# Performance work log

Measured on AMD Instinct MI355X. Metric: run time of the kernel, lower is better.

## Reference

```python
import jax, jax.numpy as jnp
import numpy as np

N, K, C, H = 8192, 32, 192, 6
HD = C // H                       # head dim = 32
SCALE = HD ** -0.5
POS_BND = int(0.8 * K)            # 25 (OctFormer RPE: 0.8*patch_size*dilation**0.5, dilation=1)
RPE_NUM = 2 * POS_BND + 1         # 51
HID = 4 * C                       # mlp hidden


def setup_inputs() -> dict:
    key = jax.random.key(0)
    ks = jax.random.split(key, 18)
    w = lambda k, sh: (jax.random.normal(k, sh, jnp.float32) * 0.02)
    data = jax.random.normal(ks[0], (N, K, C), jnp.float32)
    # rel_pos: integer xyz offsets between points in a window, roughly in [-32, 32)
    rel_pos = jax.random.randint(ks[1], (N, K, K, 3), 0, 64, jnp.int32) - 32
    mask = jnp.where(jax.random.uniform(ks[2], (N, K, K)) < 0.05, -1e9, 0.0).astype(jnp.float32)
    return {
        "data": data,
        "mask": mask,
        "rel_pos": rel_pos,
        "ln1_g": jnp.ones((C,), jnp.float32),
        "ln1_b": jnp.zeros((C,), jnp.float32),
        "qkv_w": w(ks[3], (C, 3 * C)),
        "qkv_b": jnp.zeros((3 * C,), jnp.float32),
        "rpe_table": w(ks[4], (3 * RPE_NUM, H)),
        "proj_w": w(ks[5], (C, C)),
        "proj_b": jnp.zeros((C,), jnp.float32),
        "ln2_g": jnp.ones((C,), jnp.float32),
        "ln2_b": jnp.zeros((C,), jnp.float32),
        "mlp_w1": w(ks[6], (C, HID)),
        "mlp_b1": jnp.zeros((HID,), jnp.float32),
        "mlp_w2": w(ks[7], (HID, C)),
        "mlp_b2": jnp.zeros((C,), jnp.float32),
    }


def _layernorm(x, g, b):
    m = x.mean(-1, keepdims=True)
    v = ((x - m) ** 2).mean(-1, keepdims=True)
    return (x - m) * jax.lax.rsqrt(v + 1e-5) * g + b


def reference(data, mask, rel_pos, ln1_g, ln1_b, qkv_w, qkv_b, rpe_table,
              proj_w, proj_b, ln2_g, ln2_b, mlp_w1, mlp_b1, mlp_w2, mlp_b2):
    # --- windowed attention (OctreeAttention) ---
    x = _layernorm(data, ln1_g, ln1_b)                      # (N,K,C)
    qkv = (x @ qkv_w + qkv_b).reshape(N, K, 3, H, HD)
    qkv = qkv.transpose(2, 0, 3, 1, 4)                      # (3,N,H,K,HD)
    q, k, v = qkv[0] * SCALE, qkv[1], qkv[2]
    attn = jnp.einsum('nhqd,nhkd->nhqk', q, k)              # (N,H,K,K)
    # RPE: clamp xyz offsets, index per-axis rows of the table, sum over xyz
    idx = jnp.clip(rel_pos, -POS_BND, POS_BND) + POS_BND + jnp.arange(3, dtype=rel_pos.dtype) * RPE_NUM
    rpe = rpe_table[idx].sum(axis=3)                        # (N,K,K,H)
    attn = attn + rpe.transpose(0, 3, 1, 2) + mask[:, None, :, :]
    attn = jax.nn.softmax(attn, axis=-1)
    out = jnp.einsum('nhqk,nhkd->nqhd', attn, v).reshape(N, K, C)
    out = out @ proj_w + proj_b
    data = data + out                                       # residual (gamma1=1, drop_path=0)
    # --- MLP ---
    y = _layernorm(data, ln2_g, ln2_b)
    y = jax.nn.gelu(y @ mlp_w1 + mlp_b1, approximate=False) @ mlp_w2 + mlp_b2
    return data + y
```

## Files before the change

### kernel.cpp

```cpp
#include <hip/hip_runtime.h>
#include <hip/hip_bf16.h>
#include <cmath>


#define KW    32
#define CD    192
#define NH    6
#define HID   768
#define SCALE 0.17677669529663687f

typedef short short8 __attribute__((ext_vector_type(8)));
typedef float f32x4  __attribute__((ext_vector_type(4)));
typedef unsigned short u16;

#define FB_QKV  0
#define FB_PROJ 216
#define FB_MLP1 288
#define FB_MLP2 576
#define NFRAG   864
#define WS_BYTES (NFRAG * 512 * 2)

__device__ __forceinline__ u16 f2bb(float v) {
  __hip_bfloat16 h = __float2bfloat16(v);
  return *(u16*)&h;
}
__device__ __forceinline__ float bb2f(u16 b) {
  union { float f; unsigned u; } x; x.u = ((unsigned)b) << 16; return x.f;
}

__global__ __launch_bounds__(256) void pack_weights(
    const float* __restrict__ qkv_w, const float* __restrict__ proj_w,
    const float* __restrict__ mlp_w1, const float* __restrict__ mlp_w2,
    u16* __restrict__ ws)
{
  const int idx  = blockIdx.x * 256 + threadIdx.x;
  const int f    = idx >> 6;
  const int lane = idx & 63;
  const float* src; int N, KB, fl;
  if (f < FB_PROJ)      { src = qkv_w;  N = 576; KB = 6;  fl = f; }
  else if (f < FB_MLP1) { src = proj_w; N = 192; KB = 6;  fl = f - FB_PROJ; }
  else if (f < FB_MLP2) { src = mlp_w1; N = 768; KB = 6;  fl = f - FB_MLP1; }
  else                  { src = mlp_w2; N = 192; KB = 24; fl = f - FB_MLP2; }
  const int nt = fl / KB, kb = fl % KB;
  const int k0 = kb * 32 + (lane >> 4) * 8;
  const int n  = nt * 16 + (lane & 15);
  u16* dst = ws + ((size_t)(f * 64 + lane)) * 8;
  #pragma unroll
  for (int j = 0; j < 8; ++j) dst[j] = f2bb(src[(size_t)(k0 + j) * N + n]);
}

__global__ __launch_bounds__(512, 4) void octformer_mfma(
    const float* __restrict__ data, const float* __restrict__ mask,
    const int* __restrict__ rel_pos,
    const float* __restrict__ ln1_g, const float* __restrict__ ln1_b,
    const float* __restrict__ qkv_b, const float* __restrict__ rpe_table,
    const float* __restrict__ proj_b,
    const float* __restrict__ ln2_g, const float* __restrict__ ln2_b,
    const float* __restrict__ mlp_b1, const float* __restrict__ mlp_b2,
    const u16* __restrict__ wsb, float* __restrict__ out)
{
  __shared__ __align__(16) u16 s_x[64][200];
  __shared__ __align__(16) u16 s_qkv[64][200];
  __shared__ __align__(16) u16 s_ao[64][200];

  const int tid  = threadIdx.x;
  const int n0   = blockIdx.x * 2;
  const size_t base = (size_t)blockIdx.x * (2 * KW * CD);

  const int wv   = tid >> 6;
  const int lane = tid & 63;
  const int l15  = lane & 15;
  const int quad = lane >> 4;

  const int rg = tid >> 5;
  const int c0 = tid & 31;

  const int mh   = wv >> 2;
  const int nsub = wv & 3;

  const int hh   = wv & 1;
  const int w_at = (wv >> 1) & 1;
  const int rth  = wv >> 2;

  const f32x4 zed = {0.f, 0.f, 0.f, 0.f};

  float res[4][6];
  #pragma unroll
  for (int i = 0; i < 4; ++i) {
    const int r = rg * 4 + i;
    float s = 0.f, q = 0.f;
    #pragma unroll
    for (int j = 0; j < 6; ++j) {
      const float v = data[base + r * CD + c0 + 32 * j];
      res[i][j] = v; s += v; q += v * v;
    }
    #pragma unroll
    for (int m = 16; m >= 1; m >>= 1) { s += __shfl_xor(s, m); q += __shfl_xor(q, m); }
    const float mean = s * (1.0f / CD);
    const float rstd = rsqrtf(q * (1.0f / CD) - mean * mean + 1e-5f);
    #pragma unroll
    for (int j = 0; j < 6; ++j) {
      const int c = c0 + 32 * j;
      s_x[r][c] = f2bb((res[i][j] - mean) * rstd * ln1_g[c] + ln1_b[c]);
    }
  }

  unsigned pidx[2][4];
  #pragma unroll
  for (int ct = 0; ct < 2; ++ct)
    #pragma unroll
    for (int i = 0; i < 4; ++i) {
      const int r = rth * 16 + quad * 4 + i;
      const int c = ct * 16 + l15;
      const size_t g = ((size_t)(n0 + w_at) * KW + r) * KW + c;
      const int* rp = rel_pos + 3 * g;
      int i0 = rp[0]; i0 = i0 < -25 ? -25 : (i0 > 25 ? 25 : i0); i0 += 25;
      int i1 = rp[1]; i1 = i1 < -25 ? -25 : (i1 > 25 ? 25 : i1); i1 += 76;
      int i2 = rp[2]; i2 = i2 < -25 ? -25 : (i2 > 25 ? 25 : i2); i2 += 127;
      const unsigned mb = (mask[g] < -0.5f) ? (1u << 24) : 0u;
      pidx[ct][i] = (unsigned)i0 | ((unsigned)i1 << 8) | ((unsigned)i2 << 16) | mb;
    }
  __syncthreads();

  for (int hp = 0; hp < 3; ++hp) {
    {
      f32x4 acc[3][2];
      #pragma unroll
      for (int ni = 0; ni < 3; ++ni)
        #pragma unroll
        for (int mi = 0; mi < 2; ++mi) acc[ni][mi] = zed;
      for (int kb = 0; kb < 6; ++kb) {
        short8 a[2];
        #pragma unroll
        for (int mi = 0; mi < 2; ++mi)
          a[mi] = *(const short8*)&s_x[(mh * 2 + mi) * 16 + l15][kb * 32 + quad * 8];
        #pragma unroll
        for (int ni = 0; ni < 3; ++ni) {
          const int lnt = nsub + 4 * ni, part = lnt >> 2, sub = lnt & 3;
          const int gnt = part * 12 + hp * 4 + sub;
          const short8 b = *(const short8*)(wsb + ((size_t)((FB_QKV + gnt * 6 + kb) * 64 + lane)) * 8);
          #pragma unroll
          for (int mi = 0; mi < 2; ++mi)
            acc[ni][mi] = __builtin_amdgcn_mfma_f32_16x16x32_bf16(a[mi], b, acc[ni][mi], 0, 0, 0);
        }
      }
      #pragma unroll
      for (int ni = 0; ni < 3; ++ni) {
        const int lnt = nsub + 4 * ni, part = lnt >> 2, sub = lnt & 3;
        const int gnt = part * 12 + hp * 4 + sub;
        const float bias = qkv_b[gnt * 16 + l15];
        if (part < 2) {
          #pragma unroll
          for (int mi = 0; mi < 2; ++mi)
            #pragma unroll
            for (int i = 0; i < 4; ++i) {
              float v = acc[ni][mi][i] + bias;
              if (part == 0) v *= SCALE;
              s_qkv[(mh * 2 + mi) * 16 + quad * 4 + i][part * 64 + sub * 16 + l15] = f2bb(v);
            }
        } else {
          const int vr = (sub >> 1) * 32 + (sub & 1) * 16 + l15;
          #pragma unroll
          for (int mi = 0; mi < 2; ++mi)
            #pragma unroll
            for (int i = 0; i < 4; ++i) {
              const int gr = (mh * 2 + mi) * 16 + quad * 4 + i;
              s_qkv[vr][128 + (gr >> 5) * 32 + (gr & 31)] = f2bb(acc[ni][mi][i] + bias);
            }
        }
      }
    }
    __syncthreads();

    {
      const int h = hp * 2 + hh;
      const int rbase = w_at * 32;
      const short8 qf  = *(const short8*)&s_qkv[rbase + rth * 16 + l15][hh * 32 + quad * 8];
      const short8 kf0 = *(const short8*)&s_qkv[rbase + l15][64 + hh * 32 + quad * 8];
      const short8 kf1 = *(const short8*)&s_qkv[rbase + 16 + l15][64 + hh * 32 + quad * 8];
      const f32x4 sa0 = __builtin_amdgcn_mfma_f32_16x16x32_bf16(qf, kf0, zed, 0, 0, 0);
      const f32x4 sa1 = __builtin_amdgcn_mfma_f32_16x16x32_bf16(qf, kf1, zed, 0, 0, 0);
      float S0[4], S1[4];
      #pragma unroll
      for (int i = 0; i < 4; ++i) {
        unsigned p = pidx[0][i];
        float b = rpe_table[(p & 255u) * NH + h]
                + rpe_table[((p >> 8) & 255u) * NH + h]
                + rpe_table[((p >> 16) & 255u) * NH + h];
        if (p >> 24) b -= 1e9f;
        S0[i] = sa0[i] + b;
        p = pidx[1][i];
        b = rpe_table[(p & 255u) * NH + h]
          + rpe_table[((p >> 8) & 255u) * NH + h]
          + rpe_table[((p >> 16) & 255u) * NH + h];
        if (p >> 24) b -= 1e9f;
        S1[i] = sa1[i] + b;
      }
      #pragma unroll
      for (int i = 0; i < 4; ++i) {
        float mx = fmaxf(S0[i], S1[i]);
        #pragma unroll
        for (int m = 8; m >= 1; m >>= 1) mx = fmaxf(mx, __shfl_xor(mx, m));
        const float e0 = __expf(S0[i] - mx);
        const float e1 = __expf(S1[i] - mx);
        float sm = e0 + e1;
        #pragma unroll
        for (int m = 8; m >= 1; m >>= 1) sm += __shfl_xor(sm, m);
        const float inv = 1.0f / sm;
        const int r = rbase + rth * 16 + quad * 4 + i;
        s_qkv[r][hh * 32 + l15]      = f2bb(e0 * inv);
        s_qkv[r][hh * 32 + 16 + l15] = f2bb(e1 * inv);
      }
      const short8 pf  = *(const short8*)&s_qkv[rbase + rth * 16 + l15][hh * 32 + quad * 8];
      const short8 vf0 = *(const short8*)&s_qkv[hh * 32 + l15][128 + w_at * 32 + quad * 8];
      const short8 vf1 = *(const short8*)&s_qkv[hh * 32 + 16 + l15][128 + w_at * 32 + quad * 8];
      const f32x4 o0 = __builtin_amdgcn_mfma_f32_16x16x32_bf16(pf, vf0, zed, 0, 0, 0);
      const f32x4 o1 = __builtin_amdgcn_mfma_f32_16x16x32_bf16(pf, vf1, zed, 0, 0, 0);
      #pragma unroll
      for (int i = 0; i < 4; ++i) {
        const int r = rbase + rth * 16 + quad * 4 + i;
        s_ao[r][h * 32 + l15]      = f2bb(o0[i]);
        s_ao[r][h * 32 + 16 + l15] = f2bb(o1[i]);
      }
    }
    __syncthreads();
  }

  {
    f32x4 acc[3][2];
    #pragma unroll
    for (int ni = 0; ni < 3; ++ni)
      #pragma unroll
      for (int mi = 0; mi < 2; ++mi) acc[ni][mi] = zed;
    for (int kb = 0; kb < 6; ++kb) {
      short8 a[2];
      #pragma unroll
      for (int mi = 0; mi < 2; ++mi)
        a[mi] = *(const short8*)&s_ao[(mh * 2 + mi) * 16 + l15][kb * 32 + quad * 8];
      #pragma unroll
      for (int ni = 0; ni < 3; ++ni) {
        const int nt = nsub + 4 * ni;
        const short8 b = *(const short8*)(wsb + ((size_t)((FB_PROJ + nt * 6 + kb) * 64 + lane)) * 8);
        #pragma unroll
        for (int mi = 0; mi < 2; ++mi)
          acc[ni][mi] = __builtin_amdgcn_mfma_f32_16x16x32_bf16(a[mi], b, acc[ni][mi], 0, 0, 0);
      }
    }
    #pragma unroll
    for (int ni = 0; ni < 3; ++ni) {
      const int nt = nsub + 4 * ni;
      const float bias = proj_b[nt * 16 + l15];
      #pragma unroll
      for (int mi = 0; mi < 2; ++mi)
        #pragma unroll
        for (int i = 0; i < 4; ++i)
          s_x[(mh * 2 + mi) * 16 + quad * 4 + i][nt * 16 + l15] = f2bb(acc[ni][mi][i] + bias);
    }
  }
  __syncthreads();

  #pragma unroll
  for (int i = 0; i < 4; ++i) {
    const int r = rg * 4 + i;
    float s = 0.f, q = 0.f;
    #pragma unroll
    for (int j = 0; j < 6; ++j) {
      res[i][j] += bb2f(s_x[r][c0 + 32 * j]);
      s += res[i][j]; q += res[i][j] * res[i][j];
    }
    #pragma unroll
    for (int m = 16; m >= 1; m >>= 1) { s += __shfl_xor(s, m); q += __shfl_xor(q, m); }
    const float mean = s * (1.0f / CD);
    const float rstd = rsqrtf(q * (1.0f / CD) - mean * mean + 1e-5f);
    #pragma unroll
    for (int j = 0; j < 6; ++j) {
      const int c = c0 + 32 * j;
      s_x[r][c] = f2bb((res[i][j] - mean) * rstd * ln2_g[c] + ln2_b[c]);
    }
  }
  __syncthreads();

  {
    f32x4 y[3][2];
    #pragma unroll
    for (int ni = 0; ni < 3; ++ni)
      #pragma unroll
      for (int mi = 0; mi < 2; ++mi) y[ni][mi] = zed;

    for (int cc = 0; cc < 4; ++cc) {
      {
        f32x4 acc[3][2];
        #pragma unroll
        for (int ni = 0; ni < 3; ++ni)
          #pragma unroll
          for (int mi = 0; mi < 2; ++mi) acc[ni][mi] = zed;
        for (int kb = 0; kb < 6; ++kb) {
          short8 a[2];
          #pragma unroll
          for (int mi = 0; mi < 2; ++mi)
            a[mi] = *(const short8*)&s_x[(mh * 2 + mi) * 16 + l15][kb * 32 + quad * 8];
          #pragma unroll
          for (int ni = 0; ni < 3; ++ni) {
            const int gnt = cc * 12 + nsub + 4 * ni;
            const short8 b = *(const short8*)(wsb + ((size_t)((FB_MLP1 + gnt * 6 + kb) * 64 + lane)) * 8);
            #pragma unroll
            for (int mi = 0; mi < 2; ++mi)
              acc[ni][mi] = __builtin_amdgcn_mfma_f32_16x16x32_bf16(a[mi], b, acc[ni][mi], 0, 0, 0);
          }
        }
        #pragma unroll
        for (int ni = 0; ni < 3; ++ni) {
          const int lnt = nsub + 4 * ni;
          const float b1 = mlp_b1[(cc * 12 + lnt) * 16 + l15];
          #pragma unroll
          for (int mi = 0; mi < 2; ++mi)
            #pragma unroll
            for (int i = 0; i < 4; ++i) {
              const float v = acc[ni][mi][i] + b1;
              const float gel = 0.5f * v * (1.0f + erff(v * 0.70710678118654752f));
              s_qkv[(mh * 2 + mi) * 16 + quad * 4 + i][lnt * 16 + l15] = f2bb(gel);
            }
        }
      }
      __syncthreads();

      for (int kb = 0; kb < 6; ++kb) {
        short8 a[2];
        #pragma unroll
        for (int mi = 0; mi < 2; ++mi)
          a[mi] = *(const short8*)&s_qkv[(mh * 2 + mi) * 16 + l15][kb * 32 + quad * 8];
        #pragma unroll
        for (int ni = 0; ni < 3; ++ni) {
          const int nt = nsub + 4 * ni;
          const short8 b = *(const short8*)(wsb + ((size_t)((FB_MLP2 + nt * 24 + cc * 6 + kb) * 64 + lane)) * 8);
          #pragma unroll
          for (int mi = 0; mi < 2; ++mi)
            y[ni][mi] = __builtin_amdgcn_mfma_f32_16x16x32_bf16(a[mi], b, y[ni][mi], 0, 0, 0);
        }
      }
      __syncthreads();
    }

    #pragma unroll
    for (int ni = 0; ni < 3; ++ni) {
      const int nt = nsub + 4 * ni;
      const float b2 = mlp_b2[nt * 16 + l15];
      #pragma unroll
      for (int mi = 0; mi < 2; ++mi)
        #pragma unroll
        for (int i = 0; i < 4; ++i)
          s_x[(mh * 2 + mi) * 16 + quad * 4 + i][nt * 16 + l15] = f2bb(y[ni][mi][i] + b2);
    }
  }
  __syncthreads();

  #pragma unroll
  for (int i = 0; i < 4; ++i) {
    const int r = rg * 4 + i;
    #pragma unroll
    for (int j = 0; j < 6; ++j)
      out[base + r * CD + c0 + 32 * j] = res[i][j] + bb2f(s_x[r][c0 + 32 * j]);
  }
}

__global__ __launch_bounds__(256) void octformer_scalar(
    const float* __restrict__ data, const float* __restrict__ mask, const int* __restrict__ rel_pos,
    const float* __restrict__ ln1_g, const float* __restrict__ ln1_b,
    const float* __restrict__ qkv_w, const float* __restrict__ qkv_b, const float* __restrict__ rpe_table,
    const float* __restrict__ proj_w, const float* __restrict__ proj_b,
    const float* __restrict__ ln2_g, const float* __restrict__ ln2_b,
    const float* __restrict__ mlp_w1, const float* __restrict__ mlp_b1,
    const float* __restrict__ mlp_w2, const float* __restrict__ mlp_b2,
    float* __restrict__ out)
{
  const int n = blockIdx.x, tid = threadIdx.x;
  __shared__ float s_x[KW][CD];
  __shared__ float s_ao[KW][CD];
  __shared__ float s_q[KW][33];
  __shared__ float s_k[KW][33];
  __shared__ float s_p[KW][33];
  const size_t base = (size_t)n * (KW * CD);
  const int r0 = (tid >> 5) << 2, c0 = tid & 31;
  float res[4][6];
  #pragma unroll
  for (int i = 0; i < 4; ++i)
    #pragma unroll
    for (int j = 0; j < 6; ++j) res[i][j] = data[base + (r0 + i) * CD + c0 + 32 * j];
  #pragma unroll
  for (int i = 0; i < 4; ++i) {
    float s = 0.f, q = 0.f;
    #pragma unroll
    for (int j = 0; j < 6; ++j) { s += res[i][j]; q += res[i][j] * res[i][j]; }
    #pragma unroll
    for (int m = 16; m >= 1; m >>= 1) { s += __shfl_xor(s, m); q += __shfl_xor(q, m); }
    const float mean = s / CD, rstd = rsqrtf(q / CD - mean * mean + 1e-5f);
    #pragma unroll
    for (int j = 0; j < 6; ++j) {
      const int c = c0 + 32 * j;
      s_x[r0 + i][c] = (res[i][j] - mean) * rstd * ln1_g[c] + ln1_b[c];
    }
  }
  __syncthreads();
  for (int h = 0; h < NH; ++h) {
    const int qc = h * 32 + c0, kc = CD + h * 32 + c0;
    float aq[4] = {0,0,0,0}, ak[4] = {0,0,0,0};
    for (int kk = 0; kk < CD; ++kk) {
      const float wq = qkv_w[kk * 576 + qc], wk = qkv_w[kk * 576 + kc];
      #pragma unroll
      for (int i = 0; i < 4; ++i) { const float a = s_x[r0 + i][kk]; aq[i] += a * wq; ak[i] += a * wk; }
    }
    #pragma unroll
    for (int i = 0; i < 4; ++i) {
      s_q[r0 + i][c0] = (aq[i] + qkv_b[qc]) * SCALE;
      s_k[r0 + i][c0] = ak[i] + qkv_b[kc];
    }
    __syncthreads();
    {
      float ac[4] = {0,0,0,0};
      #pragma unroll
      for (int d = 0; d < 32; ++d) {
        const float kb = s_k[c0][d];
        #pragma unroll
        for (int i = 0; i < 4; ++i) ac[i] += s_q[r0 + i][d] * kb;
      }
      #pragma unroll
      for (int i = 0; i < 4; ++i) {
        const size_t g = ((size_t)(n * KW + r0 + i)) * KW + c0;
        const int* rp = rel_pos + 3 * g;
        float rpe = 0.f;
        #pragma unroll
        for (int a = 0; a < 3; ++a) {
          int ix = rp[a]; ix = ix < -25 ? -25 : (ix > 25 ? 25 : ix);
          rpe += rpe_table[(ix + 25 + 51 * a) * NH + h];
        }
        s_p[r0 + i][c0] = ac[i] + rpe + mask[g];
      }
    }
    __syncthreads();
    {
      const int r = tid >> 3, sb = tid & 7;
      float v0 = s_p[r][sb], v1 = s_p[r][sb + 8], v2 = s_p[r][sb + 16], v3 = s_p[r][sb + 24];
      float mx = fmaxf(fmaxf(v0, v1), fmaxf(v2, v3));
      mx = fmaxf(mx, __shfl_xor(mx, 1)); mx = fmaxf(mx, __shfl_xor(mx, 2)); mx = fmaxf(mx, __shfl_xor(mx, 4));
      v0 = __expf(v0 - mx); v1 = __expf(v1 - mx); v2 = __expf(v2 - mx); v3 = __expf(v3 - mx);
      float sm = v0 + v1 + v2 + v3;
      sm += __shfl_xor(sm, 1); sm += __shfl_xor(sm, 2); sm += __shfl_xor(sm, 4);
      const float inv = 1.0f / sm;
      s_p[r][sb] = v0 * inv; s_p[r][sb + 8] = v1 * inv; s_p[r][sb + 16] = v2 * inv; s_p[r][sb + 24] = v3 * inv;
    }
    __syncthreads();
    {
      const int vc = 2 * CD + h * 32 + c0;
      float av[4] = {0,0,0,0};
      for (int kk = 0; kk < CD; ++kk) {
        const float wvv = qkv_w[kk * 576 + vc];
        #pragma unroll
        for (int i = 0; i < 4; ++i) av[i] += s_x[r0 + i][kk] * wvv;
      }
      #pragma unroll
      for (int i = 0; i < 4; ++i) s_q[r0 + i][c0] = av[i] + qkv_b[vc];
    }
    __syncthreads();
    {
      float ao[4] = {0,0,0,0};
      #pragma unroll
      for (int j = 0; j < KW; ++j) {
        const float vb = s_q[j][c0];
        #pragma unroll
        for (int i = 0; i < 4; ++i) ao[i] += s_p[r0 + i][j] * vb;
      }
      #pragma unroll
      for (int i = 0; i < 4; ++i) s_ao[r0 + i][h * 32 + c0] = ao[i];
    }
    __syncthreads();
  }
  {
    float acc[4][6];
    #pragma unroll
    for (int j = 0; j < 6; ++j) {
      const float pb = proj_b[c0 + 32 * j];
      #pragma unroll
      for (int i = 0; i < 4; ++i) acc[i][j] = pb;
    }
    for (int kk = 0; kk < CD; ++kk) {
      float a[4];
      #pragma unroll
      for (int i = 0; i < 4; ++i) a[i] = s_ao[r0 + i][kk];
      #pragma unroll
      for (int j = 0; j < 6; ++j) {
        const float w = proj_w[kk * CD + c0 + 32 * j];
        #pragma unroll
        for (int i = 0; i < 4; ++i) acc[i][j] += a[i] * w;
      }
    }
    #pragma unroll
    for (int j = 0; j < 6; ++j)
      #pragma unroll
      for (int i = 0; i < 4; ++i) res[i][j] += acc[i][j];
  }
  __syncthreads();
  #pragma unroll
  for (int i = 0; i < 4; ++i) {
    float s = 0.f, q = 0.f;
    #pragma unroll
    for (int j = 0; j < 6; ++j) { s += res[i][j]; q += res[i][j] * res[i][j]; }
    #pragma unroll
    for (int m = 16; m >= 1; m >>= 1) { s += __shfl_xor(s, m); q += __shfl_xor(q, m); }
    const float mean = s / CD, rstd = rsqrtf(q / CD - mean * mean + 1e-5f);
    #pragma unroll
    for (int j = 0; j < 6; ++j) {
      const int c = c0 + 32 * j;
      s_x[r0 + i][c] = (res[i][j] - mean) * rstd * ln2_g[c] + ln2_b[c];
    }
  }
  __syncthreads();
  {
    float y[4][6];
    #pragma unroll
    for (int j = 0; j < 6; ++j) {
      const float bb = mlp_b2[c0 + 32 * j];
      #pragma unroll
      for (int i = 0; i < 4; ++i) y[i][j] = bb;
    }
    for (int cc = 0; cc < 4; ++cc) {
      {
        float acc[4][6];
        #pragma unroll
        for (int j = 0; j < 6; ++j) {
          const float b1 = mlp_b1[cc * CD + c0 + 32 * j];
          #pragma unroll
          for (int i = 0; i < 4; ++i) acc[i][j] = b1;
        }
        for (int kk = 0; kk < CD; ++kk) {
          float a[4];
          #pragma unroll
          for (int i = 0; i < 4; ++i) a[i] = s_x[r0 + i][kk];
          #pragma unroll
          for (int j = 0; j < 6; ++j) {
            const float w = mlp_w1[kk * HID + cc * CD + c0 + 32 * j];
            #pragma unroll
            for (int i = 0; i < 4; ++i) acc[i][j] += a[i] * w;
          }
        }
        #pragma unroll
        for (int j = 0; j < 6; ++j)
          #pragma unroll
          for (int i = 0; i < 4; ++i) {
            const float x = acc[i][j];
            s_ao[r0 + i][c0 + 32 * j] = 0.5f * x * (1.0f + erff(x * 0.70710678118654752f));
          }
      }
      __syncthreads();
      for (int kk = 0; kk < CD; ++kk) {
        float a[4];
        #pragma unroll
        for (int i = 0; i < 4; ++i) a[i] = s_ao[r0 + i][kk];
        #pragma unroll
        for (int j = 0; j < 6; ++j) {
          const float w = mlp_w2[(cc * CD + kk) * CD + c0 + 32 * j];
          #pragma unroll
          for (int i = 0; i < 4; ++i) y[i][j] += a[i] * w;
        }
      }
      __syncthreads();
    }
    #pragma unroll
    for (int i = 0; i < 4; ++i)
      #pragma unroll
      for (int j = 0; j < 6; ++j)
        out[base + (r0 + i) * CD + c0 + 32 * j] = res[i][j] + y[i][j];
  }
}

extern "C" void kernel_launch(void* const* d_in, const int* in_sizes, int n_in,
                              void* d_out, int out_size, void* d_ws, size_t ws_size,
                              hipStream_t stream) {
  (void)in_sizes; (void)n_in; (void)out_size;
  const float* data   = (const float*)d_in[0];
  const float* maskp  = (const float*)d_in[1];
  const int*   relp   = (const int*)d_in[2];
  const float* ln1g   = (const float*)d_in[3];
  const float* ln1b   = (const float*)d_in[4];
  const float* qkvw   = (const float*)d_in[5];
  const float* qkvb   = (const float*)d_in[6];
  const float* rpet   = (const float*)d_in[7];
  const float* projw  = (const float*)d_in[8];
  const float* projb  = (const float*)d_in[9];
  const float* ln2g   = (const float*)d_in[10];
  const float* ln2b   = (const float*)d_in[11];
  const float* mlpw1  = (const float*)d_in[12];
  const float* mlpb1  = (const float*)d_in[13];
  const float* mlpw2  = (const float*)d_in[14];
  const float* mlpb2  = (const float*)d_in[15];
  float* outp = (float*)d_out;

  if (ws_size >= (size_t)WS_BYTES) {
    u16* ws = (u16*)d_ws;
    pack_weights<<<dim3(NFRAG / 4), dim3(256), 0, stream>>>(qkvw, projw, mlpw1, mlpw2, ws);
    octformer_mfma<<<dim3(4096), dim3(512), 0, stream>>>(
        data, maskp, relp, ln1g, ln1b, qkvb, rpet, projb, ln2g, ln2b, mlpb1, mlpb2, ws, outp);
  } else {
    octformer_scalar<<<dim3(8192), dim3(256), 0, stream>>>(
        data, maskp, relp, ln1g, ln1b, qkvw, qkvb, rpet, projw, projb,
        ln2g, ln2b, mlpw1, mlpb1, mlpw2, mlpb2, outp);
  }
}
```

Measured before the change: 1.234 ms.

## Process one window per 256-thread block instead of two per 512-thread block

Switches the fused MFMA kernel from two windows per 512-thread block to one window per 256-thread block, doubling the grid. The shared-memory tiles are halved and the wave-to-tile mapping for the QKV, attention, projection and MLP stages is reworked so each of the four waves owns one column subset over all 32 rows. The aim is smaller blocks, lower LDS use per block and more resident blocks per CU to hide latency. In exchange, each block reads the packed weight fragments for only half as many rows, so weight traffic per output row doubles.

```diff
diff --git a/kernel.cpp b/kernel.cpp
--- a/kernel.cpp
+++ b/kernel.cpp
@@ -49,7 +49,7 @@
   for (int j = 0; j < 8; ++j) dst[j] = f2bb(src[(size_t)(k0 + j) * N + n]);
 }
 
-__global__ __launch_bounds__(512, 4) void octformer_mfma(
+__global__ __launch_bounds__(256, 4) void octformer_mfma(
     const float* __restrict__ data, const float* __restrict__ mask,
     const int* __restrict__ rel_pos,
     const float* __restrict__ ln1_g, const float* __restrict__ ln1_b,
@@ -59,13 +59,13 @@
     const float* __restrict__ mlp_b1, const float* __restrict__ mlp_b2,
     const u16* __restrict__ wsb, float* __restrict__ out)
 {
-  __shared__ __align__(16) u16 s_x[64][200];
-  __shared__ __align__(16) u16 s_qkv[64][200];
-  __shared__ __align__(16) u16 s_ao[64][200];
+  __shared__ __align__(16) u16 s_x[32][200];
+  __shared__ __align__(16) u16 s_qkv[32][200];
+  __shared__ __align__(16) u16 s_ao[32][200];
 
   const int tid  = threadIdx.x;
-  const int n0   = blockIdx.x * 2;
-  const size_t base = (size_t)blockIdx.x * (2 * KW * CD);
+  const int n0   = blockIdx.x;
+  const size_t base = (size_t)n0 * (KW * CD);
 
   const int wv   = tid >> 6;
   const int lane = tid & 63;
@@ -75,12 +75,8 @@
   const int rg = tid >> 5;
   const int c0 = tid & 31;
 
-  const int mh   = wv >> 2;
-  const int nsub = wv & 3;
-
   const int hh   = wv & 1;
-  const int w_at = (wv >> 1) & 1;
-  const int rth  = wv >> 2;
+  const int rth  = wv >> 1;
 
   const f32x4 zed = {0.f, 0.f, 0.f, 0.f};
 
@@ -112,7 +108,7 @@
     for (int i = 0; i < 4; ++i) {
       const int r = rth * 16 + quad * 4 + i;
       const int c = ct * 16 + l15;
-      const size_t g = ((size_t)(n0 + w_at) * KW + r) * KW + c;
+      const size_t g = ((size_t)n0 * KW + r) * KW + c;
       const int* rp = rel_pos + 3 * g;
       int i0 = rp[0]; i0 = i0 < -25 ? -25 : (i0 > 25 ? 25 : i0); i0 += 25;
       int i1 = rp[1]; i1 = i1 < -25 ? -25 : (i1 > 25 ? 25 : i1); i1 += 76;
@@ -133,11 +129,10 @@
         short8 a[2];
         #pragma unroll
         for (int mi = 0; mi < 2; ++mi)
-          a[mi] = *(const short8*)&s_x[(mh * 2 + mi) * 16 + l15][kb * 32 + quad * 8];
+          a[mi] = *(const short8*)&s_x[mi * 16 + l15][kb * 32 + quad * 8];
         #pragma unroll
         for (int ni = 0; ni < 3; ++ni) {
-          const int lnt = nsub + 4 * ni, part = lnt >> 2, sub = lnt & 3;
-          const int gnt = part * 12 + hp * 4 + sub;
+          const int gnt = ni * 12 + hp * 4 + wv;
           const short8 b = *(const short8*)(wsb + ((size_t)((FB_QKV + gnt * 6 + kb) * 64 + lane)) * 8);
           #pragma unroll
           for (int mi = 0; mi < 2; ++mi)
@@ -146,26 +141,26 @@
       }
       #pragma unroll
       for (int ni = 0; ni < 3; ++ni) {
-        const int lnt = nsub + 4 * ni, part = lnt >> 2, sub = lnt & 3;
-        const int gnt = part * 12 + hp * 4 + sub;
+        const int gnt = ni * 12 + hp * 4 + wv;
         const float bias = qkv_b[gnt * 16 + l15];
-        if (part < 2) {
+        if (ni < 2) {
           #pragma unroll
           for (int mi = 0; mi < 2; ++mi)
             #pragma unroll
             for (int i = 0; i < 4; ++i) {
               float v = acc[ni][mi][i] + bias;
-              if (part == 0) v *= SCALE;
-              s_qkv[(mh * 2 + mi) * 16 + quad * 4 + i][part * 64 + sub * 16 + l15] = f2bb(v);
+              if (ni == 0) v *= SCALE;
+              s_qkv[mi * 16 + quad * 4 + i][ni * 64 + wv * 16 + l15] = f2bb(v);
             }
         } else {
-          const int vr = (sub >> 1) * 32 + (sub & 1) * 16 + l15;
+          const int hv = wv >> 1;
+          const int dr = (wv & 1) * 16 + l15;
           #pragma unroll
           for (int mi = 0; mi < 2; ++mi)
             #pragma unroll
             for (int i = 0; i < 4; ++i) {
-              const int gr = (mh * 2 + mi) * 16 + quad * 4 + i;
-              s_qkv[vr][128 + (gr >> 5) * 32 + (gr & 31)] = f2bb(acc[ni][mi][i] + bias);
+              const int key = mi * 16 + quad * 4 + i;
+              s_qkv[dr][128 + hv * 32 + key] = f2bb(acc[ni][mi][i] + bias);
             }
         }
       }
@@ -174,10 +169,9 @@
 
     {
       const int h = hp * 2 + hh;
-      const int rbase = w_at * 32;
-      const short8 qf  = *(const short8*)&s_qkv[rbase + rth * 16 + l15][hh * 32 + quad * 8];
-      const short8 kf0 = *(const short8*)&s_qkv[rbase + l15][64 + hh * 32 + quad * 8];
-      const short8 kf1 = *(const short8*)&s_qkv[rbase + 16 + l15][64 + hh * 32 + quad * 8];
+      const short8 qf  = *(const short8*)&s_qkv[rth * 16 + l15][hh * 32 + quad * 8];
+      const short8 kf0 = *(const short8*)&s_qkv[l15][64 + hh * 32 + quad * 8];
+      const short8 kf1 = *(const short8*)&s_qkv[16 + l15][64 + hh * 32 + quad * 8];
       const f32x4 sa0 = __builtin_amdgcn_mfma_f32_16x16x32_bf16(qf, kf0, zed, 0, 0, 0);
       const f32x4 sa1 = __builtin_amdgcn_mfma_f32_16x16x32_bf16(qf, kf1, zed, 0, 0, 0);
       float S0[4], S1[4];
@@ -207,18 +201,18 @@
         #pragma unroll
         for (int m = 8; m >= 1; m >>= 1) sm += __shfl_xor(sm, m);
         const float inv = 1.0f / sm;
-        const int r = rbase + rth * 16 + quad * 4 + i;
+        const int r = rth * 16 + quad * 4 + i;
         s_qkv[r][hh * 32 + l15]      = f2bb(e0 * inv);
         s_qkv[r][hh * 32 + 16 + l15] = f2bb(e1 * inv);
       }
-      const short8 pf  = *(const short8*)&s_qkv[rbase + rth * 16 + l15][hh * 32 + quad * 8];
-      const short8 vf0 = *(const short8*)&s_qkv[hh * 32 + l15][128 + w_at * 32 + quad * 8];
-      const short8 vf1 = *(const short8*)&s_qkv[hh * 32 + 16 + l15][128 + w_at * 32 + quad * 8];
+      const short8 pf  = *(const short8*)&s_qkv[rth * 16 + l15][hh * 32 + quad * 8];
+      const short8 vf0 = *(const short8*)&s_qkv[l15][128 + hh * 32 + quad * 8];
+      const short8 vf1 = *(const short8*)&s_qkv[16 + l15][128 + hh * 32 + quad * 8];
       const f32x4 o0 = __builtin_amdgcn_mfma_f32_16x16x32_bf16(pf, vf0, zed, 0, 0, 0);
       const f32x4 o1 = __builtin_amdgcn_mfma_f32_16x16x32_bf16(pf, vf1, zed, 0, 0, 0);
       #pragma unroll
       for (int i = 0; i < 4; ++i) {
-        const int r = rbase + rth * 16 + quad * 4 + i;
+        const int r = rth * 16 + quad * 4 + i;
         s_ao[r][h * 32 + l15]      = f2bb(o0[i]);
         s_ao[r][h * 32 + 16 + l15] = f2bb(o1[i]);
       }
@@ -236,10 +230,10 @@
       short8 a[2];
       #pragma unroll
       for (int mi = 0; mi < 2; ++mi)
-        a[mi] = *(const short8*)&s_ao[(mh * 2 + mi) * 16 + l15][kb * 32 + quad * 8];
+        a[mi] = *(const short8*)&s_ao[mi * 16 + l15][kb * 32 + quad * 8];
       #pragma unroll
       for (int ni = 0; ni < 3; ++ni) {
-        const int nt = nsub + 4 * ni;
+        const int nt = wv + 4 * ni;
         const short8 b = *(const short8*)(wsb + ((size_t)((FB_PROJ + nt * 6 + kb) * 64 + lane)) * 8);
         #pragma unroll
         for (int mi = 0; mi < 2; ++mi)
@@ -248,13 +242,13 @@
     }
     #pragma unroll
     for (int ni = 0; ni < 3; ++ni) {
-      const int nt = nsub + 4 * ni;
+      const int nt = wv + 4 * ni;
       const float bias = proj_b[nt * 16 + l15];
       #pragma unroll
       for (int mi = 0; mi < 2; ++mi)
         #pragma unroll
         for (int i = 0; i < 4; ++i)
-          s_x[(mh * 2 + mi) * 16 + quad * 4 + i][nt * 16 + l15] = f2bb(acc[ni][mi][i] + bias);
+          s_x[mi * 16 + quad * 4 + i][nt * 16 + l15] = f2bb(acc[ni][mi][i] + bias);
     }
   }
   __syncthreads();
@@ -298,10 +292,10 @@
           short8 a[2];
           #pragma unroll
           for (int mi = 0; mi < 2; ++mi)
-            a[mi] = *(const short8*)&s_x[(mh * 2 + mi) * 16 + l15][kb * 32 + quad * 8];
+            a[mi] = *(const short8*)&s_x[mi * 16 + l15][kb * 32 + quad * 8];
           #pragma unroll
           for (int ni = 0; ni < 3; ++ni) {
-            const int gnt = cc * 12 + nsub + 4 * ni;
+            const int gnt = cc * 12 + wv + 4 * ni;
             const short8 b = *(const short8*)(wsb + ((size_t)((FB_MLP1 + gnt * 6 + kb) * 64 + lane)) * 8);
             #pragma unroll
             for (int mi = 0; mi < 2; ++mi)
@@ -310,7 +304,7 @@
         }
         #pragma unroll
         for (int ni = 0; ni < 3; ++ni) {
-          const int lnt = nsub + 4 * ni;
+          const int lnt = wv + 4 * ni;
           const float b1 = mlp_b1[(cc * 12 + lnt) * 16 + l15];
           #pragma unroll
           for (int mi = 0; mi < 2; ++mi)
@@ -318,7 +312,7 @@
             for (int i = 0; i < 4; ++i) {
               const float v = acc[ni][mi][i] + b1;
               const float gel = 0.5f * v * (1.0f + erff(v * 0.70710678118654752f));
-              s_qkv[(mh * 2 + mi) * 16 + quad * 4 + i][lnt * 16 + l15] = f2bb(gel);
+              s_qkv[mi * 16 + quad * 4 + i][lnt * 16 + l15] = f2bb(gel);
             }
         }
       }
@@ -328,10 +322,10 @@
         short8 a[2];
         #pragma unroll
         for (int mi = 0; mi < 2; ++mi)
-          a[mi] = *(const short8*)&s_qkv[(mh * 2 + mi) * 16 + l15][kb * 32 + quad * 8];
+          a[mi] = *(const short8*)&s_qkv[mi * 16 + l15][kb * 32 + quad * 8];
         #pragma unroll
         for (int ni = 0; ni < 3; ++ni) {
-          const int nt = nsub + 4 * ni;
+          const int nt = wv + 4 * ni;
           const short8 b = *(const short8*)(wsb + ((size_t)((FB_MLP2 + nt * 24 + cc * 6 + kb) * 64 + lane)) * 8);
           #pragma unroll
           for (int mi = 0; mi < 2; ++mi)
@@ -343,13 +337,13 @@
 
     #pragma unroll
     for (int ni = 0; ni < 3; ++ni) {
-      const int nt = nsub + 4 * ni;
+      const int nt = wv + 4 * ni;
       const float b2 = mlp_b2[nt * 16 + l15];
       #pragma unroll
       for (int mi = 0; mi < 2; ++mi)
         #pragma unroll
         for (int i = 0; i < 4; ++i)
-          s_x[(mh * 2 + mi) * 16 + quad * 4 + i][nt * 16 + l15] = f2bb(y[ni][mi][i] + b2);
+          s_x[mi * 16 + quad * 4 + i][nt * 16 + l15] = f2bb(y[ni][mi][i] + b2);
     }
   }
   __syncthreads();
@@ -597,7 +591,7 @@
   if (ws_size >= (size_t)WS_BYTES) {
     u16* ws = (u16*)d_ws;
     pack_weights<<<dim3(NFRAG / 4), dim3(256), 0, stream>>>(qkvw, projw, mlpw1, mlpw2, ws);
-    octformer_mfma<<<dim3(4096), dim3(512), 0, stream>>>(
+    octformer_mfma<<<dim3(8192), dim3(256), 0, stream>>>(
         data, maskp, relp, ln1g, ln1b, qkvb, rpet, projb, ln2g, ln2b, mlpb1, mlpb2, ws, outp);
   } else {
     octformer_scalar<<<dim3(8192), dim3(256), 0, stream>>>(
```

Measured after the change: 1.225 ms. About the same (-0.7%).

## Split fused block kernel into separate attention and MLP kernels

Applied to the files above, without the earlier changes.

Splits the single fused kernel into an attention kernel that writes the post-attention residual to the output buffer and an MLP kernel that reads it back, applies LN2 and the MLP, and adds its result in place. This frees the residual registers and the third shared buffer in the MLP stage, which may raise occupancy. The cost is an extra global round trip of the full activation tensor and a second launch. It also drops the min-blocks hint from the launch bounds and simplifies the QKV tile index math.

```diff
diff --git a/kernel.cpp b/kernel.cpp
--- a/kernel.cpp
+++ b/kernel.cpp
@@ -49,15 +49,13 @@
   for (int j = 0; j < 8; ++j) dst[j] = f2bb(src[(size_t)(k0 + j) * N + n]);
 }
 
-__global__ __launch_bounds__(512, 4) void octformer_mfma(
+__global__ __launch_bounds__(512) void octformer_attn(
     const float* __restrict__ data, const float* __restrict__ mask,
     const int* __restrict__ rel_pos,
     const float* __restrict__ ln1_g, const float* __restrict__ ln1_b,
     const float* __restrict__ qkv_b, const float* __restrict__ rpe_table,
     const float* __restrict__ proj_b,
-    const float* __restrict__ ln2_g, const float* __restrict__ ln2_b,
-    const float* __restrict__ mlp_b1, const float* __restrict__ mlp_b2,
-    const u16* __restrict__ wsb, float* __restrict__ out)
+    const u16* __restrict__ wsb, float* __restrict__ x2)
 {
   __shared__ __align__(16) u16 s_x[64][200];
   __shared__ __align__(16) u16 s_qkv[64][200];
@@ -84,15 +82,14 @@
 
   const f32x4 zed = {0.f, 0.f, 0.f, 0.f};
 
-  float res[4][6];
   #pragma unroll
   for (int i = 0; i < 4; ++i) {
     const int r = rg * 4 + i;
-    float s = 0.f, q = 0.f;
-    #pragma unroll
-    for (int j = 0; j < 6; ++j) {
-      const float v = data[base + r * CD + c0 + 32 * j];
-      res[i][j] = v; s += v; q += v * v;
+    float v[6]; float s = 0.f, q = 0.f;
+    #pragma unroll
+    for (int j = 0; j < 6; ++j) {
+      v[j] = data[base + r * CD + c0 + 32 * j];
+      s += v[j]; q += v[j] * v[j];
     }
     #pragma unroll
     for (int m = 16; m >= 1; m >>= 1) { s += __shfl_xor(s, m); q += __shfl_xor(q, m); }
@@ -101,7 +98,7 @@
     #pragma unroll
     for (int j = 0; j < 6; ++j) {
       const int c = c0 + 32 * j;
-      s_x[r][c] = f2bb((res[i][j] - mean) * rstd * ln1_g[c] + ln1_b[c]);
+      s_x[r][c] = f2bb((v[j] - mean) * rstd * ln1_g[c] + ln1_b[c]);
     }
   }
 
@@ -136,8 +133,7 @@
           a[mi] = *(const short8*)&s_x[(mh * 2 + mi) * 16 + l15][kb * 32 + quad * 8];
         #pragma unroll
         for (int ni = 0; ni < 3; ++ni) {
-          const int lnt = nsub + 4 * ni, part = lnt >> 2, sub = lnt & 3;
-          const int gnt = part * 12 + hp * 4 + sub;
+          const int gnt = ni * 12 + hp * 4 + nsub;
           const short8 b = *(const short8*)(wsb + ((size_t)((FB_QKV + gnt * 6 + kb) * 64 + lane)) * 8);
           #pragma unroll
           for (int mi = 0; mi < 2; ++mi)
@@ -146,20 +142,19 @@
       }
       #pragma unroll
       for (int ni = 0; ni < 3; ++ni) {
-        const int lnt = nsub + 4 * ni, part = lnt >> 2, sub = lnt & 3;
-        const int gnt = part * 12 + hp * 4 + sub;
+        const int gnt = ni * 12 + hp * 4 + nsub;
         const float bias = qkv_b[gnt * 16 + l15];
-        if (part < 2) {
+        if (ni < 2) {
           #pragma unroll
           for (int mi = 0; mi < 2; ++mi)
             #pragma unroll
             for (int i = 0; i < 4; ++i) {
               float v = acc[ni][mi][i] + bias;
-              if (part == 0) v *= SCALE;
-              s_qkv[(mh * 2 + mi) * 16 + quad * 4 + i][part * 64 + sub * 16 + l15] = f2bb(v);
+              if (ni == 0) v *= SCALE;
+              s_qkv[(mh * 2 + mi) * 16 + quad * 4 + i][ni * 64 + nsub * 16 + l15] = f2bb(v);
             }
         } else {
-          const int vr = (sub >> 1) * 32 + (sub & 1) * 16 + l15;
+          const int vr = (nsub >> 1) * 32 + (nsub & 1) * 16 + l15;
           #pragma unroll
           for (int mi = 0; mi < 2; ++mi)
             #pragma unroll
@@ -262,11 +257,46 @@
   #pragma unroll
   for (int i = 0; i < 4; ++i) {
     const int r = rg * 4 + i;
-    float s = 0.f, q = 0.f;
-    #pragma unroll
-    for (int j = 0; j < 6; ++j) {
-      res[i][j] += bb2f(s_x[r][c0 + 32 * j]);
-      s += res[i][j]; q += res[i][j] * res[i][j];
+    #pragma unroll
+    for (int j = 0; j < 6; ++j) {
+      const int c = c0 + 32 * j;
+      x2[base + r * CD + c] = data[base + r * CD + c] + bb2f(s_x[r][c]);
+    }
+  }
+}
+
+__global__ __launch_bounds__(512) void octformer_mlp(
+    const float* __restrict__ ln2_g, const float* __restrict__ ln2_b,
+    const float* __restrict__ mlp_b1, const float* __restrict__ mlp_b2,
+    const u16* __restrict__ wsb, float* __restrict__ io)
+{
+  __shared__ __align__(16) u16 s_x[64][200];
+  __shared__ __align__(16) u16 s_h[64][200];
+
+  const int tid  = threadIdx.x;
+  const size_t base = (size_t)blockIdx.x * (64 * CD);
+
+  const int wv   = tid >> 6;
+  const int lane = tid & 63;
+  const int l15  = lane & 15;
+  const int quad = lane >> 4;
+
+  const int rg = tid >> 5;
+  const int c0 = tid & 31;
+
+  const int mh   = wv >> 2;
+  const int nsub = wv & 3;
+
+  const f32x4 zed = {0.f, 0.f, 0.f, 0.f};
+
+  #pragma unroll
+  for (int i = 0; i < 4; ++i) {
+    const int r = rg * 4 + i;
+    float v[6]; float s = 0.f, q = 0.f;
+    #pragma unroll
+    for (int j = 0; j < 6; ++j) {
+      v[j] = io[base + r * CD + c0 + 32 * j];
+      s += v[j]; q += v[j] * v[j];
     }
     #pragma unroll
     for (int m = 16; m >= 1; m >>= 1) { s += __shfl_xor(s, m); q += __shfl_xor(q, m); }
@@ -275,91 +305,82 @@
     #pragma unroll
     for (int j = 0; j < 6; ++j) {
       const int c = c0 + 32 * j;
-      s_x[r][c] = f2bb((res[i][j] - mean) * rstd * ln2_g[c] + ln2_b[c]);
+      s_x[r][c] = f2bb((v[j] - mean) * rstd * ln2_g[c] + ln2_b[c]);
     }
   }
   __syncthreads();
 
-  {
-    f32x4 y[3][2];
-    #pragma unroll
-    for (int ni = 0; ni < 3; ++ni)
-      #pragma unroll
-      for (int mi = 0; mi < 2; ++mi) y[ni][mi] = zed;
-
-    for (int cc = 0; cc < 4; ++cc) {
-      {
-        f32x4 acc[3][2];
-        #pragma unroll
-        for (int ni = 0; ni < 3; ++ni)
-          #pragma unroll
-          for (int mi = 0; mi < 2; ++mi) acc[ni][mi] = zed;
-        for (int kb = 0; kb < 6; ++kb) {
-          short8 a[2];
-          #pragma unroll
-          for (int mi = 0; mi < 2; ++mi)
-            a[mi] = *(const short8*)&s_x[(mh * 2 + mi) * 16 + l15][kb * 32 + quad * 8];
-          #pragma unroll
-          for (int ni = 0; ni < 3; ++ni) {
-            const int gnt = cc * 12 + nsub + 4 * ni;
-            const short8 b = *(const short8*)(wsb + ((size_t)((FB_MLP1 + gnt * 6 + kb) * 64 + lane)) * 8);
-            #pragma unroll
-            for (int mi = 0; mi < 2; ++mi)
-              acc[ni][mi] = __builtin_amdgcn_mfma_f32_16x16x32_bf16(a[mi], b, acc[ni][mi], 0, 0, 0);
-          }
-        }
-        #pragma unroll
-        for (int ni = 0; ni < 3; ++ni) {
-          const int lnt = nsub + 4 * ni;
-          const float b1 = mlp_b1[(cc * 12 + lnt) * 16 + l15];
-          #pragma unroll
-          for (int mi = 0; mi < 2; ++mi)
-            #pragma unroll
-            for (int i = 0; i < 4; ++i) {
-              const float v = acc[ni][mi][i] + b1;
-              const float gel = 0.5f * v * (1.0f + erff(v * 0.70710678118654752f));
-              s_qkv[(mh * 2 + mi) * 16 + quad * 4 + i][lnt * 16 + l15] = f2bb(gel);
-            }
-        }
-      }
-      __syncthreads();
-
+  f32x4 y[3][2];
+  #pragma unroll
+  for (int ni = 0; ni < 3; ++ni)
+    #pragma unroll
+    for (int mi = 0; mi < 2; ++mi) y[ni][mi] = zed;
+
+  for (int cc = 0; cc < 4; ++cc) {
+    {
+      f32x4 acc[3][2];
+      #pragma unroll
+      for (int ni = 0; ni < 3; ++ni)
+        #pragma unroll
+        for (int mi = 0; mi < 2; ++mi) acc[ni][mi] = zed;
       for (int kb = 0; kb < 6; ++kb) {
         short8 a[2];
         #pragma unroll
         for (int mi = 0; mi < 2; ++mi)
-          a[mi] = *(const short8*)&s_qkv[(mh * 2 + mi) * 16 + l15][kb * 32 + quad * 8];
+          a[mi] = *(const short8*)&s_x[(mh * 2 + mi) * 16 + l15][kb * 32 + quad * 8];
         #pragma unroll
         for (int ni = 0; ni < 3; ++ni) {
-          const int nt = nsub + 4 * ni;
-          const short8 b = *(const short8*)(wsb + ((size_t)((FB_MLP2 + nt * 24 + cc * 6 + kb) * 64 + lane)) * 8);
+          const int gnt = cc * 12 + nsub + 4 * ni;
+          const short8 b = *(const short8*)(wsb + ((size_t)((FB_MLP1 + gnt * 6 + kb) * 64 + lane)) * 8);
           #pragma unroll
           for (int mi = 0; mi < 2; ++mi)
-            y[ni][mi] = __builtin_amdgcn_mfma_f32_16x16x32_bf16(a[mi], b, y[ni][mi], 0, 0, 0);
+            acc[ni][mi] = __builtin_amdgcn_mfma_f32_16x16x32_bf16(a[mi], b, acc[ni][mi], 0, 0, 0);
         }
       }
-      __syncthreads();
-    }
-
-    #pragma unroll
-    for (int ni = 0; ni < 3; ++ni) {
-      const int nt = nsub + 4 * ni;
-      const float b2 = mlp_b2[nt * 16 + l15];
+      #pragma unroll
+      for (int ni = 0; ni < 3; ++ni) {
+        const int lnt = nsub + 4 * ni;
+        const float b1 = mlp_b1[(cc * 12 + lnt) * 16 + l15];
+        #pragma unroll
+        for (int mi = 0; mi < 2; ++mi)
+          #pragma unroll
+          for (int i = 0; i < 4; ++i) {
+            const float v = acc[ni][mi][i] + b1;
+            const float gel = 0.5f * v * (1.0f + erff(v * 0.70710678118654752f));
+            s_h[(mh * 2 + mi) * 16 + quad * 4 + i][lnt * 16 + l15] = f2bb(gel);
+          }
+      }
+    }
+    __syncthreads();
+
+    for (int kb = 0; kb < 6; ++kb) {
+      short8 a[2];
       #pragma unroll
       for (int mi = 0; mi < 2; ++mi)
-        #pragma unroll
-        for (int i = 0; i < 4; ++i)
-          s_x[(mh * 2 + mi) * 16 + quad * 4 + i][nt * 16 + l15] = f2bb(y[ni][mi][i] + b2);
-    }
-  }
-  __syncthreads();
-
-  #pragma unroll
-  for (int i = 0; i < 4; ++i) {
-    const int r = rg * 4 + i;
-    #pragma unroll
-    for (int j = 0; j < 6; ++j)
-      out[base + r * CD + c0 + 32 * j] = res[i][j] + bb2f(s_x[r][c0 + 32 * j]);
+        a[mi] = *(const short8*)&s_h[(mh * 2 + mi) * 16 + l15][kb * 32 + quad * 8];
+      #pragma unroll
+      for (int ni = 0; ni < 3; ++ni) {
+        const int nt = nsub + 4 * ni;
+        const short8 b = *(const short8*)(wsb + ((size_t)((FB_MLP2 + nt * 24 + cc * 6 + kb) * 64 + lane)) * 8);
+        #pragma unroll
+        for (int mi = 0; mi < 2; ++mi)
+          y[ni][mi] = __builtin_amdgcn_mfma_f32_16x16x32_bf16(a[mi], b, y[ni][mi], 0, 0, 0);
+      }
+    }
+    __syncthreads();
+  }
+
+  #pragma unroll
+  for (int ni = 0; ni < 3; ++ni) {
+    const int nt = nsub + 4 * ni;
+    const float b2 = mlp_b2[nt * 16 + l15];
+    #pragma unroll
+    for (int mi = 0; mi < 2; ++mi)
+      #pragma unroll
+      for (int i = 0; i < 4; ++i) {
+        const size_t g = base + (size_t)((mh * 2 + mi) * 16 + quad * 4 + i) * CD + nt * 16 + l15;
+        io[g] = io[g] + y[ni][mi][i] + b2;
+      }
   }
 }
 
@@ -597,8 +618,10 @@
   if (ws_size >= (size_t)WS_BYTES) {
     u16* ws = (u16*)d_ws;
     pack_weights<<<dim3(NFRAG / 4), dim3(256), 0, stream>>>(qkvw, projw, mlpw1, mlpw2, ws);
-    octformer_mfma<<<dim3(4096), dim3(512), 0, stream>>>(
-        data, maskp, relp, ln1g, ln1b, qkvb, rpet, projb, ln2g, ln2b, mlpb1, mlpb2, ws, outp);
+    octformer_attn<<<dim3(4096), dim3(512), 0, stream>>>(
+        data, maskp, relp, ln1g, ln1b, qkvb, rpet, projb, ws, outp);
+    octformer_mlp<<<dim3(4096), dim3(512), 0, stream>>>(
+        ln2g, ln2b, mlpb1, mlpb2, ws, outp);
   } else {
     octformer_scalar<<<dim3(8192), dim3(256), 0, stream>>>(
         data, maskp, relp, ln1g, ln1b, qkvw, qkvb, rpet, projw, projb,
```

Result: faster. 1.136 ms (-7.9%).
